# Kernel tuning notes

Measured on AMD Instinct MI355X. Metric: run time of the kernel, lower is better.

The kernel has to match this reference:

```python
import jax, jax.numpy as jnp
import numpy as np

C_CONST = 8.0   # RG-LRU decay constant (Griffin/Hawk)
EPS = 1e-6      # RMSNorm eps
K = 4           # causal depthwise conv kernel size


def rmsnorm(x, w):
    # x: [B,S,D]
    var = jnp.mean(x * x, axis=-1, keepdims=True)
    return x * jax.lax.rsqrt(var + EPS) * w


def causal_depthwise_conv(x, conv_w, conv_b):
    # x: [B,S,D], conv_w: [K,D], conv_b: [D]; causal (left-pad K-1)
    B, S, D = x.shape
    xp = jnp.pad(x, ((0, 0), (K - 1, 0), (0, 0)))
    out = conv_b
    for k in range(K):  # tiny fixed loop over kernel taps
        out = out + conv_w[k] * xp[:, k:k + S, :]
    return out


def rg_lru(x, Wi, Wa, lam):
    # x: [B,S,D]; diagonal linear recurrence h_t = a_t*h_{t-1} + sqrt(1-a_t^2)*(i_t*x_t)
    r = jax.nn.sigmoid(jnp.einsum('bsd,de->bse', x, Wa))   # recurrence gate
    i = jax.nn.sigmoid(jnp.einsum('bsd,de->bse', x, Wi))   # input gate
    log_a = -C_CONST * jax.nn.softplus(lam) * r            # [B,S,D]
    a = jnp.exp(log_a)
    b = jnp.sqrt(jnp.maximum(1.0 - a * a, 1e-12)) * (i * x)

    def comb(e1, e2):
        a1, b1 = e1
        a2, b2 = e2
        return (a1 * a2, a2 * b1 + b2)

    _, h = jax.lax.associative_scan(comb, (a, b), axis=1)
    return h


def setup_inputs() -> dict:
    key = jax.random.key(0)
    ks = jax.random.split(key, 16)
    B, S, D, H = 4, 2048, 1024, 4096
    s = 0.02
    return {
        'x': jax.random.normal(ks[0], (B, S, D), jnp.float32),
        'norm1_w': jnp.ones((D,), jnp.float32),
        'Wx': jax.random.normal(ks[1], (D, D), jnp.float32) * s,
        'Wy': jax.random.normal(ks[2], (D, D), jnp.float32) * s,
        'conv_w': jax.random.normal(ks[3], (K, D), jnp.float32) * s,
        'conv_b': jnp.zeros((D,), jnp.float32),
        'Wi': jax.random.normal(ks[4], (D, D), jnp.float32) * s,
        'Wa': jax.random.normal(ks[5], (D, D), jnp.float32) * s,
        'lam': jax.random.normal(ks[6], (D,), jnp.float32) * 0.5,
        'Wo': jax.random.normal(ks[7], (D, D), jnp.float32) * s,
        'norm2_w': jnp.ones((D,), jnp.float32),
        'Wg': jax.random.normal(ks[8], (D, H), jnp.float32) * s,
        'Wu': jax.random.normal(ks[9], (D, H), jnp.float32) * s,
        'Wd': jax.random.normal(ks[10], (H, D), jnp.float32) * s,
    }


def reference(x, norm1_w, Wx, Wy, conv_w, conv_b, Wi, Wa, lam, Wo,
              norm2_w, Wg, Wu, Wd):
    # --- mixing block (Hawk recurrent block) with pre-norm + residual ---
    t = rmsnorm(x, norm1_w)
    xb = jnp.einsum('bsd,de->bse', t, Wx)          # recurrence branch
    xb = causal_depthwise_conv(xb, conv_w, conv_b)
    h = rg_lru(xb, Wi, Wa, lam)
    yb = jax.nn.gelu(jnp.einsum('bsd,de->bse', t, Wy))  # gate branch
    mix = jnp.einsum('bsd,de->bse', h * yb, Wo)
    h1 = x + mix
    # --- gated MLP with pre-norm + residual ---
    u = rmsnorm(h1, norm2_w)
    ffn = jnp.einsum('bsh,hd->bsd', jax.nn.gelu(jnp.einsum('bsd,dh->bsh', u, Wg)) * jnp.einsum('bsd,dh->bsh', u, Wu), Wd)
    return h1 + ffn
```

## Files before the change

kernel.cpp:

```cpp
#include <hip/hip_runtime.h>
#include <hip/hip_bf16.h>
#include <stdint.h>

#define B_SZ   4
#define S_LEN  2048
#define D_DIM  1024
#define H_DIM  4096
#define T_TOK  (B_SZ * S_LEN)
#define NC     64
#define CL     32

typedef unsigned short u16;
typedef unsigned int   u32;
typedef __attribute__((ext_vector_type(8))) short short8;
typedef __attribute__((ext_vector_type(4))) float f32x4;

__device__ __forceinline__ float tof(u16 u) {
    union { u32 i; float f; } v; v.i = ((u32)u) << 16; return v.f;
}
__device__ __forceinline__ u16 tobf(float f) {
    union { float f; u32 i; } v; v.f = f;
    u32 x = v.i;
    return (u16)((x + 0x7FFFu + ((x >> 16) & 1u)) >> 16);
}
__device__ __forceinline__ void unp8(uint4 v, float* f) {
    f[0] = tof(v.x & 0xffff); f[1] = tof(v.x >> 16);
    f[2] = tof(v.y & 0xffff); f[3] = tof(v.y >> 16);
    f[4] = tof(v.z & 0xffff); f[5] = tof(v.z >> 16);
    f[6] = tof(v.w & 0xffff); f[7] = tof(v.w >> 16);
}

__device__ __forceinline__ float gelu_f(float x) {
    float x3 = x * x * x;
    float tin = 0.7978845608028654f * (x + 0.044715f * x3);
    float e = __expf(2.f * tin);
    float th = 1.f - 2.f / (e + 1.f);
    return 0.5f * x * (1.f + th);
}
__device__ __forceinline__ float sig_f(float x) {
    return 1.f / (1.f + __expf(-x));
}

__device__ __forceinline__ void gload16(const void* g, void* l) {
    __builtin_amdgcn_global_load_lds(
        (const __attribute__((address_space(1))) u32*)g,
        (__attribute__((address_space(3))) u32*)l,
        16, 0, 0);
}

__global__ void detect_k(const u32* __restrict__ w, int* __restrict__ flag) {
    if (blockIdx.x == 0 && threadIdx.x == 0)
        *flag = (w[0] == 0x3F800000u) ? 1 : 0;
}

__global__ __launch_bounds__(256) void prep_small(
    const void* n1w, const void* n2w, const void* cw, const void* cb,
    const void* lam, u16* n1wc, u16* n2wc, u16* cwc, u16* cbc,
    float* acoef, const int* __restrict__ flagp) {
    int i = blockIdx.x * 256 + threadIdx.x;
    bool f32 = (*flagp) != 0;
    auto rd = [&](const void* p, int j) {
        return f32 ? ((const float*)p)[j] : tof(((const u16*)p)[j]);
    };
    if (i < 1024) n1wc[i] = tobf(rd(n1w, i));
    else if (i < 2048) n2wc[i - 1024] = tobf(rd(n2w, i - 1024));
    else if (i < 6144) cwc[i - 2048] = tobf(rd(cw, i - 2048));
    else if (i < 7168) cbc[i - 6144] = tobf(rd(cb, i - 6144));
    else {
        int d = i - 7168;
        float l = rd(lam, d);
        float sp = fmaxf(l, 0.f) + log1pf(__expf(-fabsf(l)));
        acoef[d] = -8.f * sp;
    }
}

__global__ __launch_bounds__(256) void transpose_all(
    const void* Wx_, const void* Wy_, const void* Wa_, const void* Wi_,
    const void* Wo_, const void* Wd_, const void* Wg_, const void* Wu_,
    u16* WTxy, u16* WTai, u16* WTo, u16* WTd, u16* WTgu,
    const int* __restrict__ flagp) {
    const size_t DD = (size_t)D_DIM * D_DIM;
    bool f32 = (*flagp) != 0;
    int b = blockIdx.x;
    const void* W; u16* WT; int R, C, gx, ilv = 0, par = 0;
    if (b < 1024)       { W = Wx_; WT = WTxy;      R = 1024; C = 1024; gx = 32;  b -= 0; }
    else if (b < 2048)  { W = Wy_; WT = WTxy + DD; R = 1024; C = 1024; gx = 32;  b -= 1024; }
    else if (b < 3072)  { W = Wa_; WT = WTai;      R = 1024; C = 1024; gx = 32;  b -= 2048; }
    else if (b < 4096)  { W = Wi_; WT = WTai + DD; R = 1024; C = 1024; gx = 32;  b -= 3072; }
    else if (b < 5120)  { W = Wo_; WT = WTo;       R = 1024; C = 1024; gx = 32;  b -= 4096; }
    else if (b < 9216)  { W = Wd_; WT = WTd;       R = 4096; C = 1024; gx = 32;  b -= 5120; }
    else if (b < 13312) { W = Wg_; WT = WTgu;      R = 1024; C = 4096; gx = 128; b -= 9216;  ilv = 1; par = 0; }
    else                { W = Wu_; WT = WTgu;      R = 1024; C = 4096; gx = 128; b -= 13312; ilv = 1; par = 1; }
    int bx = b % gx, by = b / gx;
    __shared__ u16 tile[32][33];
    int tx = threadIdx.x & 31, ty = threadIdx.x >> 5;
    int c0 = bx * 32, r0 = by * 32;
#pragma unroll
    for (int k = 0; k < 4; k++) {
        size_t idx = (size_t)(r0 + ty + k * 8) * C + c0 + tx;
        tile[ty + k * 8][tx] = f32 ? tobf(((const float*)W)[idx])
                                   : ((const u16*)W)[idx];
    }
    __syncthreads();
#pragma unroll
    for (int k = 0; k < 4; k++) {
        int cc = c0 + ty + k * 8;
        size_t orow = ilv ? (size_t)(2 * cc + par) : (size_t)cc;
        WT[orow * R + r0 + tx] = tile[tx][ty + k * 8];
    }
}

__global__ __launch_bounds__(256) void rmsnorm_any(
    const void* __restrict__ X, const u16* __restrict__ Wt, u16* __restrict__ O,
    const int* __restrict__ flagp, int in_mode) {
    bool f32 = in_mode == 1 || (*flagp != 0);
    int row = blockIdx.x;
    int t = threadIdx.x;
    float x0, x1, x2, x3;
    if (f32) {
        float4 v = ((const float4*)((const float*)X + (size_t)row * D_DIM))[t];
        x0 = v.x; x1 = v.y; x2 = v.z; x3 = v.w;
    } else {
        uint2 pv = ((const uint2*)((const u16*)X + (size_t)row * D_DIM))[t];
        x0 = tof(pv.x & 0xffff); x1 = tof(pv.x >> 16);
        x2 = tof(pv.y & 0xffff); x3 = tof(pv.y >> 16);
    }
    float ss = x0 * x0 + x1 * x1 + x2 * x2 + x3 * x3;
#pragma unroll
    for (int off = 32; off; off >>= 1) ss += __shfl_down(ss, off, 64);
    __shared__ float red[4];
    if ((t & 63) == 0) red[t >> 6] = ss;
    __syncthreads();
    float tot = red[0] + red[1] + red[2] + red[3];
    float rs = rsqrtf(tot * (1.f / D_DIM) + 1e-6f);
    uint2 wv = ((const uint2*)Wt)[t];
    float w0 = tof(wv.x & 0xffff), w1 = tof(wv.x >> 16);
    float w2 = tof(wv.y & 0xffff), w3 = tof(wv.y >> 16);
    uint2 ov;
    ov.x = (u32)tobf(x0 * rs * w0) | ((u32)tobf(x1 * rs * w1) << 16);
    ov.y = (u32)tobf(x2 * rs * w2) | ((u32)tobf(x3 * rs * w3) << 16);
    ((uint2*)(O + (size_t)row * D_DIM))[t] = ov;
}

__global__ __launch_bounds__(256) void conv_k(
    const u16* __restrict__ xb, const u16* __restrict__ cw,
    const u16* __restrict__ cb, u16* __restrict__ xc) {
    size_t idx = (size_t)blockIdx.x * 256 + threadIdx.x;
    int dp = (int)(idx & 127);
    size_t ts = idx >> 7;
    int s = (int)(ts & (S_LEN - 1));
    int d0 = dp * 8;
    float acc[8];
    unp8(*(const uint4*)(cb + d0), acc);
    size_t base = ts * D_DIM + d0;
#pragma unroll
    for (int k = 0; k < 4; k++) {
        int sp = s + k - 3;
        if (sp >= 0) {
            float xf[8], wf[8];
            unp8(*(const uint4*)(xb + base + (ptrdiff_t)(k - 3) * D_DIM), xf);
            unp8(*(const uint4*)(cw + k * D_DIM + d0), wf);
#pragma unroll
            for (int e = 0; e < 8; e++) acc[e] += wf[e] * xf[e];
        }
    }
    uint4 ov;
    ov.x = (u32)tobf(acc[0]) | ((u32)tobf(acc[1]) << 16);
    ov.y = (u32)tobf(acc[2]) | ((u32)tobf(acc[3]) << 16);
    ov.z = (u32)tobf(acc[4]) | ((u32)tobf(acc[5]) << 16);
    ov.w = (u32)tobf(acc[6]) | ((u32)tobf(acc[7]) << 16);
    *(uint4*)(xc + base) = ov;
}

__global__ __launch_bounds__(256) void gates_chunk_k(
    const u16* __restrict__ r, const u16* __restrict__ ii, const u16* __restrict__ xc,
    const float* __restrict__ acoef, float2* __restrict__ Ap2, float2* __restrict__ Bs2) {
    int d2 = blockIdx.x * 256 + threadIdx.x;
    int c = blockIdx.y, b = blockIdx.z;
    float ac0 = acoef[d2 * 2], ac1 = acoef[d2 * 2 + 1];
    const u32* r2 = (const u32*)r;
    const u32* i2 = (const u32*)ii;
    const u32* x2 = (const u32*)xc;
    size_t base = ((size_t)b * S_LEN + c * CL) * (D_DIM / 2) + d2;
    float ap0 = 1.f, bs0 = 0.f, ap1 = 1.f, bs1 = 0.f;
    for (int tt = 0; tt < CL; tt++) {
        u32 rv = r2[base], iv = i2[base], xv = x2[base];
        float a0 = __expf(ac0 * tof(rv & 0xffff));
        float a1 = __expf(ac1 * tof(rv >> 16));
        float b0 = sqrtf(fmaxf(1.f - a0 * a0, 1e-12f)) * (tof(iv & 0xffff) * tof(xv & 0xffff));
        float b1 = sqrtf(fmaxf(1.f - a1 * a1, 1e-12f)) * (tof(iv >> 16) * tof(xv >> 16));
        ap0 *= a0; bs0 = fmaf(a0, bs0, b0);
        ap1 *= a1; bs1 = fmaf(a1, bs1, b1);
        base += D_DIM / 2;
    }
    size_t o = ((size_t)b * NC + c) * (D_DIM / 2) + d2;
    Ap2[o] = make_float2(ap0, ap1);
    Bs2[o] = make_float2(bs0, bs1);
}

__global__ __launch_bounds__(256) void carry_k(
    const float2* __restrict__ Ap2, const float2* __restrict__ Bs2,
    float2* __restrict__ carry2) {
    int d2 = blockIdx.x * 256 + threadIdx.x;
    int b = blockIdx.y;
    float2 h = make_float2(0.f, 0.f);
    for (int c = 0; c < NC; c++) {
        size_t o = ((size_t)b * NC + c) * (D_DIM / 2) + d2;
        float2 ap = Ap2[o], bs = Bs2[o];
        carry2[o] = h;
        h.x = fmaf(ap.x, h.x, bs.x);
        h.y = fmaf(ap.y, h.y, bs.y);
    }
}

__global__ __launch_bounds__(256) void apply_k(
    const u16* __restrict__ r, const u16* __restrict__ ii, const u16* __restrict__ xc,
    const float* __restrict__ acoef, const float2* __restrict__ carry2,
    const u16* __restrict__ yb, u16* __restrict__ g) {
    int d2 = blockIdx.x * 256 + threadIdx.x;
    int c = blockIdx.y, b = blockIdx.z;
    float ac0 = acoef[d2 * 2], ac1 = acoef[d2 * 2 + 1];
    float2 h = carry2[((size_t)b * NC + c) * (D_DIM / 2) + d2];
    const u32* r2 = (const u32*)r;
    const u32* i2 = (const u32*)ii;
    const u32* x2 = (const u32*)xc;
    const u32* y2 = (const u32*)yb;
    u32* g2 = (u32*)g;
    size_t base = ((size_t)b * S_LEN + c * CL) * (D_DIM / 2) + d2;
    for (int tt = 0; tt < CL; tt++) {
        u32 rv = r2[base], iv = i2[base], xv = x2[base], yv = y2[base];
        float a0 = __expf(ac0 * tof(rv & 0xffff));
        float a1 = __expf(ac1 * tof(rv >> 16));
        float b0 = sqrtf(fmaxf(1.f - a0 * a0, 1e-12f)) * (tof(iv & 0xffff) * tof(xv & 0xffff));
        float b1 = sqrtf(fmaxf(1.f - a1 * a1, 1e-12f)) * (tof(iv >> 16) * tof(xv >> 16));
        h.x = fmaf(a0, h.x, b0);
        h.y = fmaf(a1, h.y, b1);
        g2[base] = (u32)tobf(h.x * tof(yv & 0xffff)) |
                   ((u32)tobf(h.y * tof(yv >> 16)) << 16);
        base += D_DIM / 2;
    }
}

enum { EPI_NONE = 0, EPI_GELU = 1, EPI_SIG = 2, EPI_RESID = 3, EPI_MUL = 4 };

template <int E>
__device__ __forceinline__ float epi_apply(float v, const void* aux, size_t idx,
                                           bool auxF32) {
    if (E == EPI_GELU) return gelu_f(v);
    if (E == EPI_SIG) return sig_f(v);
    if (E == EPI_RESID) {
        float a = auxF32 ? ((const float*)aux)[idx] : tof(((const u16*)aux)[idx]);
        return v + a;
    }
    if (E == EPI_MUL) {
        float a = auxF32 ? ((const float*)aux)[idx] : tof(((const u16*)aux)[idx]);
        return v * a;
    }
    return v;
}

#define BK 32

template <int BM, int BN, int WMD, int WND, int EPI0, int EPI1, bool OUTF32,
          bool SWZ, bool GLU>
__global__ __launch_bounds__(WMD * WND * 64, 4) void gemm_db(
    const u16* __restrict__ A, const u16* __restrict__ BT,
    void* __restrict__ C0v, void* __restrict__ C1v, const void* __restrict__ aux,
    const int* __restrict__ flagp, int aux_mode,
    int M, int N, int K, int halfN) {
    constexpr int T  = WMD * WND * 64;
    constexpr int MR = BM / WMD;
    constexpr int NR = BN / WND;
    constexpr int MI = MR / 16;
    constexpr int NJ = NR / 16;
    constexpr int RPR = T / 4;

    __shared__ __align__(16) u16 As[2][BM * BK];
    __shared__ __align__(16) u16 Bs[2][BN * BK];

    const int t = threadIdx.x;
    const int lane = t & 63;
    const int w = t >> 6;
    const int wm = w / WND, wn = w % WND;
    const int quad = lane >> 4, l16 = lane & 15;

    int mt, nt;
    if (SWZ) {
        int GN = gridDim.x;
        int L = blockIdx.y * GN + blockIdx.x;
        int per = (GN * gridDim.y) >> 3;
        int id = (L & 7) * per + (L >> 3);
        mt = id / GN; nt = id - mt * GN;
    } else {
        mt = blockIdx.y; nt = blockIdx.x;
    }
    const int m0 = mt * BM;
    const int n0 = nt * BN;

    const int srow = t >> 2;
    const int cbg  = (t & 3) ^ ((srow >> 1) & 3);
    const u16* ag = A + (size_t)(m0 + srow) * K + cbg * 8;
    const u16* bg = BT + (size_t)(n0 + srow) * K + cbg * 8;
    const size_t rstep = (size_t)RPR * K;

    f32x4 acc[MI][NJ];
#pragma unroll
    for (int i = 0; i < MI; i++)
#pragma unroll
        for (int j = 0; j < NJ; j++) acc[i][j] = (f32x4){0.f, 0.f, 0.f, 0.f};

    const int pcb = (quad ^ ((l16 >> 1) & 3)) * 8;

    auto STAGE = [&](int s, int kt) {
        const u16* a = ag + (size_t)kt * BK;
        const u16* b = bg + (size_t)kt * BK;
        char* lA = (char*)&As[s][0] + t * 16;
        char* lB = (char*)&Bs[s][0] + t * 16;
#pragma unroll
        for (int rr = 0; rr < BM / RPR; rr++)
            gload16(a + rr * rstep, lA + rr * (RPR * 64));
#pragma unroll
        for (int rr = 0; rr < BN / RPR; rr++)
            gload16(b + rr * rstep, lB + rr * (RPR * 64));
    };
    auto COMPUTE = [&](int s) {
        short8 af[MI], bf[NJ];
#pragma unroll
        for (int i = 0; i < MI; i++)
            af[i] = *(const short8*)&As[s][(wm * MR + i * 16 + l16) * BK + pcb];
#pragma unroll
        for (int j = 0; j < NJ; j++)
            bf[j] = *(const short8*)&Bs[s][(wn * NR + j * 16 + l16) * BK + pcb];
#pragma unroll
        for (int i = 0; i < MI; i++)
#pragma unroll
            for (int j = 0; j < NJ; j++)
                acc[i][j] = __builtin_amdgcn_mfma_f32_16x16x32_bf16(
                    af[i], bf[j], acc[i][j], 0, 0, 0);
    };

    const int NT = K >> 5;
    STAGE(0, 0);
    __syncthreads();
    for (int kt = 0; kt < NT; kt += 2) {
        STAGE(1, kt + 1);
        COMPUTE(0);
        __syncthreads();
        if (kt + 2 < NT) STAGE(0, kt + 2);
        COMPUTE(1);
        __syncthreads();
    }

    const bool auxF32 = (aux_mode == 2) || (aux_mode == 1 && *flagp != 0);
    const int side = (!GLU && n0 >= halfN) ? 1 : 0;
    void* Cv = side ? C1v : C0v;

#pragma unroll
    for (int i = 0; i < MI; i++) {
        int mbase = m0 + wm * MR + i * 16 + quad * 4;
#pragma unroll
        for (int j = 0; j < NJ; j++) {
            int ncol = n0 - side * halfN + wn * NR + j * 16 + l16;
#pragma unroll
            for (int rr = 0; rr < 4; rr++) {
                float v = acc[i][j][rr];
                if (GLU) {
                    float o = __shfl_xor(v, 1);
                    bool odd = (l16 & 1) != 0;
                    float gg = odd ? o : v;
                    float uu = odd ? v : o;
                    float res = gelu_f(gg) * uu;
                    if (!odd)
                        ((u16*)C0v)[(size_t)(mbase + rr) * halfN + (ncol >> 1)]
                            = tobf(res);
                } else {
                    size_t idx = (size_t)(mbase + rr) * halfN + ncol;
                    v = side ? epi_apply<EPI1>(v, aux, idx, auxF32)
                             : epi_apply<EPI0>(v, aux, idx, auxF32);
                    if (OUTF32) ((float*)Cv)[idx] = v;
                    else        ((u16*)Cv)[idx] = tobf(v);
                }
            }
        }
    }
}

extern "C" void kernel_launch(void* const* d_in, const int* in_sizes, int n_in,
                              void* d_out, int out_size, void* d_ws, size_t ws_size,
                              hipStream_t stream) {
    const void* x      = d_in[0];
    const void* n1w    = d_in[1];
    const void* Wx     = d_in[2];
    const void* Wy     = d_in[3];
    const void* conv_w = d_in[4];
    const void* conv_b = d_in[5];
    const void* Wi     = d_in[6];
    const void* Wa     = d_in[7];
    const void* lam    = d_in[8];
    const void* Wo     = d_in[9];
    const void* n2w    = d_in[10];
    const void* Wg     = d_in[11];
    const void* Wu     = d_in[12];
    const void* Wd     = d_in[13];
    float* out = (float*)d_out;

    char* ws = (char*)d_ws;
    auto alloc = [&](size_t bytes) {
        char* p = ws;
        ws += (bytes + 255) & ~(size_t)255;
        return p;
    };
    const size_t DD = (size_t)D_DIM * D_DIM;
    const size_t TD = (size_t)T_TOK * D_DIM * 2;
    const size_t TH = (size_t)T_TOK * H_DIM * 2;

    int*  dflag  = (int*)alloc(256);
    u16*  n1wc   = (u16*)alloc(D_DIM * 2);
    u16*  n2wc   = (u16*)alloc(D_DIM * 2);
    u16*  cwc    = (u16*)alloc(4 * D_DIM * 2);
    u16*  cbc    = (u16*)alloc(D_DIM * 2);
    float* acoef = (float*)alloc(D_DIM * 4);
    float2* Ap2    = (float2*)alloc((size_t)B_SZ * NC * D_DIM * 4);
    float2* Bs2    = (float2*)alloc((size_t)B_SZ * NC * D_DIM * 4);
    float2* carry2 = (float2*)alloc((size_t)B_SZ * NC * D_DIM * 4);
    u16* WTxy = (u16*)alloc(2 * DD * 2);
    u16* WTai = (u16*)alloc(2 * DD * 2);
    u16* WTo  = (u16*)alloc(DD * 2);
    u16* WTd  = (u16*)alloc((size_t)D_DIM * H_DIM * 2);
    u16* WTgu = (u16*)alloc((size_t)D_DIM * H_DIM * 2 * 2);
    u16* T0  = (u16*)alloc(TD);
    u16* T1  = (u16*)alloc(TD);
    u16* T2  = (u16*)alloc(TD);
    u16* T3  = (u16*)alloc(TD);
    u16* T4  = (u16*)alloc(TD);
    u16* ggb = (u16*)alloc(TH);
    float* h1f = (float*)alloc((size_t)T_TOK * D_DIM * 4);

    dim3 b256(256);

    detect_k<<<dim3(1), dim3(64), 0, stream>>>((const u32*)n1w, dflag);
    prep_small<<<dim3(32), b256, 0, stream>>>(n1w, n2w, conv_w, conv_b, lam,
                                              n1wc, n2wc, cwc, cbc, acoef, dflag);
    transpose_all<<<dim3(17408), b256, 0, stream>>>(
        Wx, Wy, Wa, Wi, Wo, Wd, Wg, Wu, WTxy, WTai, WTo, WTd, WTgu, dflag);

    rmsnorm_any<<<dim3(T_TOK), b256, 0, stream>>>(x, n1wc, T2, dflag, 0);

    gemm_db<128, 128, 2, 2, EPI_NONE, EPI_GELU, false, false, false>
        <<<dim3(2 * D_DIM / 128, T_TOK / 128), b256, 0, stream>>>(
        T2, WTxy, T1, T3, nullptr, dflag, 0, T_TOK, 2 * D_DIM, D_DIM, D_DIM);

    conv_k<<<dim3(T_TOK * D_DIM / 8 / 256), b256, 0, stream>>>(T1, cwc, cbc, T0);

    gemm_db<128, 128, 2, 2, EPI_SIG, EPI_SIG, false, false, false>
        <<<dim3(2 * D_DIM / 128, T_TOK / 128), b256, 0, stream>>>(
        T0, WTai, T4, T2, nullptr, dflag, 0, T_TOK, 2 * D_DIM, D_DIM, D_DIM);

    gates_chunk_k<<<dim3(2, NC, B_SZ), b256, 0, stream>>>(T4, T2, T0, acoef, Ap2, Bs2);
    carry_k<<<dim3(2, B_SZ), b256, 0, stream>>>(Ap2, Bs2, carry2);
    apply_k<<<dim3(2, NC, B_SZ), b256, 0, stream>>>(T4, T2, T0, acoef, carry2, T3, T4);

    gemm_db<128, 128, 2, 2, EPI_RESID, EPI_RESID, true, false, false>
        <<<dim3(D_DIM / 128, T_TOK / 128), b256, 0, stream>>>(
        T4, WTo, h1f, h1f, x, dflag, 1, T_TOK, D_DIM, D_DIM, D_DIM);

    rmsnorm_any<<<dim3(T_TOK), b256, 0, stream>>>(h1f, n2wc, T1, dflag, 1);

    gemm_db<128, 128, 2, 2, EPI_NONE, EPI_NONE, false, false, true>
        <<<dim3(2 * H_DIM / 128, T_TOK / 128), b256, 0, stream>>>(
        T1, WTgu, ggb, ggb, nullptr, dflag, 0, T_TOK, 2 * H_DIM, D_DIM, H_DIM);

    gemm_db<128, 128, 2, 2, EPI_RESID, EPI_RESID, true, true, false>
        <<<dim3(D_DIM / 128, T_TOK / 128), b256, 0, stream>>>(
        ggb, WTd, out, out, h1f, dflag, 2, T_TOK, D_DIM, H_DIM, D_DIM);
}
```

Before: 685.1 us.

## Overlap MLP weight transposes with scan kernels and simplify GLU epilogue

Splits the big weight-transpose launch so the Wg/Wu and Wd transposes run as extra blocks inside the low-occupancy scan kernels (gates and apply), filling idle CUs. The Wg/Wu interleave changes from per-column to 16-column groups, which lets the GLU epilogue pair accumulator fragments directly instead of using cross-lane shuffles. It also changes the grid swizzle mapping in the GEMM. This adds complexity, and the new interleave has to match the GEMM column pairing exactly for the results to be correct.

Measured after the change: 656.5 us. -4.2%, faster.

```diff
diff --git a/kernel.cpp b/kernel.cpp
--- a/kernel.cpp
+++ b/kernel.cpp
@@ -74,24 +74,9 @@
     }
 }
 
-__global__ __launch_bounds__(256) void transpose_all(
-    const void* Wx_, const void* Wy_, const void* Wa_, const void* Wi_,
-    const void* Wo_, const void* Wd_, const void* Wg_, const void* Wu_,
-    u16* WTxy, u16* WTai, u16* WTo, u16* WTd, u16* WTgu,
-    const int* __restrict__ flagp) {
-    const size_t DD = (size_t)D_DIM * D_DIM;
-    bool f32 = (*flagp) != 0;
-    int b = blockIdx.x;
-    const void* W; u16* WT; int R, C, gx, ilv = 0, par = 0;
-    if (b < 1024)       { W = Wx_; WT = WTxy;      R = 1024; C = 1024; gx = 32;  b -= 0; }
-    else if (b < 2048)  { W = Wy_; WT = WTxy + DD; R = 1024; C = 1024; gx = 32;  b -= 1024; }
-    else if (b < 3072)  { W = Wa_; WT = WTai;      R = 1024; C = 1024; gx = 32;  b -= 2048; }
-    else if (b < 4096)  { W = Wi_; WT = WTai + DD; R = 1024; C = 1024; gx = 32;  b -= 3072; }
-    else if (b < 5120)  { W = Wo_; WT = WTo;       R = 1024; C = 1024; gx = 32;  b -= 4096; }
-    else if (b < 9216)  { W = Wd_; WT = WTd;       R = 4096; C = 1024; gx = 32;  b -= 5120; }
-    else if (b < 13312) { W = Wg_; WT = WTgu;      R = 1024; C = 4096; gx = 128; b -= 9216;  ilv = 1; par = 0; }
-    else                { W = Wu_; WT = WTgu;      R = 1024; C = 4096; gx = 128; b -= 13312; ilv = 1; par = 1; }
-    int bx = b % gx, by = b / gx;
+__device__ __forceinline__ void tr_tile32(
+    const void* W, u16* WT, int R, int C, int bx, int by, bool f32,
+    int ilv16, int par) {
     __shared__ u16 tile[32][33];
     int tx = threadIdx.x & 31, ty = threadIdx.x >> 5;
     int c0 = bx * 32, r0 = by * 32;
@@ -105,9 +90,25 @@
 #pragma unroll
     for (int k = 0; k < 4; k++) {
         int cc = c0 + ty + k * 8;
-        size_t orow = ilv ? (size_t)(2 * cc + par) : (size_t)cc;
+        size_t orow = ilv16 ? (size_t)(((cc >> 4) << 5) + par * 16 + (cc & 15))
+                            : (size_t)cc;
         WT[orow * R + r0 + tx] = tile[tx][ty + k * 8];
     }
+}
+
+__global__ __launch_bounds__(256) void transpose5(
+    const void* Wx_, const void* Wy_, const void* Wa_, const void* Wi_,
+    const void* Wo_, u16* WTxy, u16* WTai, u16* WTo,
+    const int* __restrict__ flagp) {
+    const size_t DD = (size_t)D_DIM * D_DIM;
+    int b = blockIdx.x;
+    const void* W; u16* WT;
+    if (b < 1024)       { W = Wx_; WT = WTxy; }
+    else if (b < 2048)  { W = Wy_; WT = WTxy + DD; b -= 1024; }
+    else if (b < 3072)  { W = Wa_; WT = WTai;      b -= 2048; }
+    else if (b < 4096)  { W = Wi_; WT = WTai + DD; b -= 3072; }
+    else                { W = Wo_; WT = WTo;       b -= 4096; }
+    tr_tile32(W, WT, 1024, 1024, b % 32, b / 32, (*flagp) != 0, 0, 0);
 }
 
 __global__ __launch_bounds__(256) void rmsnorm_any(
@@ -172,11 +173,22 @@
     *(uint4*)(xc + base) = ov;
 }
 
-__global__ __launch_bounds__(256) void gates_chunk_k(
+__global__ __launch_bounds__(256) void gates_fused(
     const u16* __restrict__ r, const u16* __restrict__ ii, const u16* __restrict__ xc,
-    const float* __restrict__ acoef, float2* __restrict__ Ap2, float2* __restrict__ Bs2) {
-    int d2 = blockIdx.x * 256 + threadIdx.x;
-    int c = blockIdx.y, b = blockIdx.z;
+    const float* __restrict__ acoef, float2* __restrict__ Ap2, float2* __restrict__ Bs2,
+    const void* Wg_, const void* Wu_, u16* __restrict__ WTgu,
+    const int* __restrict__ flagp) {
+    int bid = blockIdx.x;
+    if (bid >= 512) {
+        int tb = bid - 512;
+        int par = tb >= 4096 ? 1 : 0;
+        if (par) tb -= 4096;
+        tr_tile32(par ? Wu_ : Wg_, WTgu, 1024, 4096, tb % 128, tb / 128,
+                  (*flagp) != 0, 1, par);
+        return;
+    }
+    int d2 = (bid & 1) * 256 + threadIdx.x;
+    int c = (bid >> 1) & 63, b = bid >> 7;
     float ac0 = acoef[d2 * 2], ac1 = acoef[d2 * 2 + 1];
     const u32* r2 = (const u32*)r;
     const u32* i2 = (const u32*)ii;
@@ -213,12 +225,19 @@
     }
 }
 
-__global__ __launch_bounds__(256) void apply_k(
+__global__ __launch_bounds__(256) void apply_fused(
     const u16* __restrict__ r, const u16* __restrict__ ii, const u16* __restrict__ xc,
     const float* __restrict__ acoef, const float2* __restrict__ carry2,
-    const u16* __restrict__ yb, u16* __restrict__ g) {
-    int d2 = blockIdx.x * 256 + threadIdx.x;
-    int c = blockIdx.y, b = blockIdx.z;
+    const u16* __restrict__ yb, u16* __restrict__ g,
+    const void* Wd_, u16* __restrict__ WTd, const int* __restrict__ flagp) {
+    int bid = blockIdx.x;
+    if (bid >= 512) {
+        int tb = bid - 512;
+        tr_tile32(Wd_, WTd, 4096, 1024, tb % 32, tb / 32, (*flagp) != 0, 0, 0);
+        return;
+    }
+    int d2 = (bid & 1) * 256 + threadIdx.x;
+    int c = (bid >> 1) & 63, b = bid >> 7;
     float ac0 = acoef[d2 * 2], ac1 = acoef[d2 * 2 + 1];
     float2 h = carry2[((size_t)b * NC + c) * (D_DIM / 2) + d2];
     const u32* r2 = (const u32*)r;
@@ -286,11 +305,12 @@
 
     int mt, nt;
     if (SWZ) {
-        int GN = gridDim.x;
-        int L = blockIdx.y * GN + blockIdx.x;
-        int per = (GN * gridDim.y) >> 3;
-        int id = (L & 7) * per + (L >> 3);
-        mt = id / GN; nt = id - mt * GN;
+        int GX = gridDim.x;
+        int gxc = GX >> 3;
+        int L = blockIdx.y * GX + blockIdx.x;
+        int c = L & 7, q = L >> 3;
+        mt = q / gxc;
+        nt = c * gxc + (q - mt * gxc);
     } else {
         mt = blockIdx.y; nt = blockIdx.x;
     }
@@ -352,7 +372,25 @@
     }
 
     const bool auxF32 = (aux_mode == 2) || (aux_mode == 1 && *flagp != 0);
-    const int side = (!GLU && n0 >= halfN) ? 1 : 0;
+
+    if (GLU) {
+#pragma unroll
+        for (int i = 0; i < MI; i++) {
+            int mbase = m0 + wm * MR + i * 16 + quad * 4;
+#pragma unroll
+            for (int jp = 0; jp < NJ / 2; jp++) {
+                int ocol = (n0 >> 1) + wn * (NR / 2) + jp * 16 + l16;
+#pragma unroll
+                for (int rr = 0; rr < 4; rr++) {
+                    float res = gelu_f(acc[i][2 * jp][rr]) * acc[i][2 * jp + 1][rr];
+                    ((u16*)C0v)[(size_t)(mbase + rr) * halfN + ocol] = tobf(res);
+                }
+            }
+        }
+        return;
+    }
+
+    const int side = (n0 >= halfN) ? 1 : 0;
     void* Cv = side ? C1v : C0v;
 
 #pragma unroll
@@ -363,23 +401,12 @@
             int ncol = n0 - side * halfN + wn * NR + j * 16 + l16;
 #pragma unroll
             for (int rr = 0; rr < 4; rr++) {
+                size_t idx = (size_t)(mbase + rr) * halfN + ncol;
                 float v = acc[i][j][rr];
-                if (GLU) {
-                    float o = __shfl_xor(v, 1);
-                    bool odd = (l16 & 1) != 0;
-                    float gg = odd ? o : v;
-                    float uu = odd ? v : o;
-                    float res = gelu_f(gg) * uu;
-                    if (!odd)
-                        ((u16*)C0v)[(size_t)(mbase + rr) * halfN + (ncol >> 1)]
-                            = tobf(res);
-                } else {
-                    size_t idx = (size_t)(mbase + rr) * halfN + ncol;
-                    v = side ? epi_apply<EPI1>(v, aux, idx, auxF32)
-                             : epi_apply<EPI0>(v, aux, idx, auxF32);
-                    if (OUTF32) ((float*)Cv)[idx] = v;
-                    else        ((u16*)Cv)[idx] = tobf(v);
-                }
+                v = side ? epi_apply<EPI1>(v, aux, idx, auxF32)
+                         : epi_apply<EPI0>(v, aux, idx, auxF32);
+                if (OUTF32) ((float*)Cv)[idx] = v;
+                else        ((u16*)Cv)[idx] = tobf(v);
             }
         }
     }
@@ -441,8 +468,8 @@
     detect_k<<<dim3(1), dim3(64), 0, stream>>>((const u32*)n1w, dflag);
     prep_small<<<dim3(32), b256, 0, stream>>>(n1w, n2w, conv_w, conv_b, lam,
                                               n1wc, n2wc, cwc, cbc, acoef, dflag);
-    transpose_all<<<dim3(17408), b256, 0, stream>>>(
-        Wx, Wy, Wa, Wi, Wo, Wd, Wg, Wu, WTxy, WTai, WTo, WTd, WTgu, dflag);
+    transpose5<<<dim3(5120), b256, 0, stream>>>(
+        Wx, Wy, Wa, Wi, Wo, WTxy, WTai, WTo, dflag);
 
     rmsnorm_any<<<dim3(T_TOK), b256, 0, stream>>>(x, n1wc, T2, dflag, 0);
 
@@ -456,9 +483,11 @@
         <<<dim3(2 * D_DIM / 128, T_TOK / 128), b256, 0, stream>>>(
         T0, WTai, T4, T2, nullptr, dflag, 0, T_TOK, 2 * D_DIM, D_DIM, D_DIM);
 
-    gates_chunk_k<<<dim3(2, NC, B_SZ), b256, 0, stream>>>(T4, T2, T0, acoef, Ap2, Bs2);
+    gates_fused<<<dim3(512 + 2 * 4096), b256, 0, stream>>>(
+        T4, T2, T0, acoef, Ap2, Bs2, Wg, Wu, WTgu, dflag);
     carry_k<<<dim3(2, B_SZ), b256, 0, stream>>>(Ap2, Bs2, carry2);
-    apply_k<<<dim3(2, NC, B_SZ), b256, 0, stream>>>(T4, T2, T0, acoef, carry2, T3, T4);
+    apply_fused<<<dim3(512 + 4096), b256, 0, stream>>>(
+        T4, T2, T0, acoef, carry2, T3, T4, Wd, WTd, dflag);
 
     gemm_db<128, 128, 2, 2, EPI_RESID, EPI_RESID, true, false, false>
         <<<dim3(D_DIM / 128, T_TOK / 128), b256, 0, stream>>>(
```
